# Optimization experiments

Hardware: AMD Instinct MI355X
Metric: run time of the kernel (lower is better)

The kernel has to match this reference:

```python
import jax, jax.numpy as jnp
import numpy as np

B, L, D_MODEL = 2, 4096, 256
EXPAND = 2
D_INNER = EXPAND * D_MODEL
D_STATE = 16
D_CONV = 4
DT_RANK = max(1, D_MODEL // 16)


def setup_inputs() -> dict:
    key = jax.random.key(0)
    ks = jax.random.split(key, 8)
    s = 0.02
    return {
        "x": jax.random.normal(ks[0], (B, L, D_MODEL), jnp.float32),
        "in_proj_w": jax.random.normal(ks[1], (D_MODEL, 2 * D_INNER), jnp.float32) * s,
        "conv_w": jax.random.normal(ks[2], (D_INNER, D_CONV), jnp.float32) * 0.1,
        "conv_b": jnp.zeros((D_INNER,), jnp.float32),
        "x_proj_w": jax.random.normal(ks[3], (D_INNER, DT_RANK + 2 * D_STATE), jnp.float32) * s,
        "dt_proj_w": jax.random.normal(ks[4], (DT_RANK, D_INNER), jnp.float32) * (DT_RANK ** -0.5),
        "dt_proj_b": jnp.log(jnp.expm1(jnp.full((D_INNER,), 0.01, jnp.float32))),
        "A_log": jnp.log(jnp.tile(jnp.arange(1, D_STATE + 1, dtype=jnp.float32), (D_INNER, 1))),
        "D": jnp.ones((D_INNER,), jnp.float32),
        "out_proj_w": jax.random.normal(ks[5], (D_INNER, D_MODEL), jnp.float32) * s,
        "ln_gamma": jnp.ones((D_MODEL,), jnp.float32),
        "ln_beta": jnp.zeros((D_MODEL,), jnp.float32),
    }


def _mamba(x, in_proj_w, conv_w, conv_b, x_proj_w, dt_proj_w, dt_proj_b, A_log, D, out_proj_w):
    b = x.shape[0]
    xz = x @ in_proj_w                       # [B,L,2*d_inner]
    u, z = jnp.split(xz, 2, axis=-1)
    # depthwise causal conv over time
    u_pad = jnp.pad(u, ((0, 0), (D_CONV - 1, 0), (0, 0)))
    kern = conv_w.T[:, None, :]              # [D_CONV, 1, D_INNER]
    u_conv = jax.lax.conv_general_dilated(
        u_pad, kern, (1,), 'VALID',
        dimension_numbers=('NHC', 'HIO', 'NHC'),
        feature_group_count=D_INNER) + conv_b
    u_conv = jax.nn.silu(u_conv)             # [B,L,d_inner]
    dbl = u_conv @ x_proj_w
    dt, Bm, Cm = jnp.split(dbl, [DT_RANK, DT_RANK + D_STATE], axis=-1)
    delta = jax.nn.softplus(dt @ dt_proj_w + dt_proj_b)   # [B,L,d_inner]
    A = -jnp.exp(A_log)                                    # [d_inner,d_state]
    dA = jnp.exp(delta[..., None] * A)                     # [B,L,di,ds]
    dBu = delta[..., None] * Bm[:, :, None, :] * u_conv[..., None]

    def step(h, inputs):
        dA_t, dBu_t, C_t = inputs
        h = dA_t * h + dBu_t                 # [B,di,ds]
        y = jnp.einsum('bdn,bn->bd', h, C_t)
        return h, y

    h0 = jnp.zeros((b, D_INNER, D_STATE), u_conv.dtype)
    _, ys = jax.lax.scan(step, h0,
                         (dA.transpose(1, 0, 2, 3),
                          dBu.transpose(1, 0, 2, 3),
                          Cm.transpose(1, 0, 2)))
    y = ys.transpose(1, 0, 2) + u_conv * D
    y = y * jax.nn.silu(z)
    return y @ out_proj_w


def reference(x, in_proj_w, conv_w, conv_b, x_proj_w, dt_proj_w, dt_proj_b,
              A_log, D, out_proj_w, ln_gamma, ln_beta):
    y = x + _mamba(x, in_proj_w, conv_w, conv_b, x_proj_w, dt_proj_w,
                   dt_proj_b, A_log, D, out_proj_w)
    mu = jnp.mean(y, axis=-1, keepdims=True)
    var = jnp.var(y, axis=-1, keepdims=True)
    return (y - mu) / jnp.sqrt(var + 1e-5) * ln_gamma + ln_beta
```

## Files before the change

### kernel.cpp

```cpp
#include <hip/hip_runtime.h>
#include <math.h>

constexpr int BATCH  = 2;
constexpr int LSEQ   = 4096;
constexpr int DMODEL = 256;
constexpr int DINNER = 512;
constexpr int NST    = 16;
constexpr int MROWS  = BATCH * LSEQ;
constexpr int NCH    = 256;
constexpr int TCH    = LSEQ / NCH;
constexpr float LOG2E = 1.44269504088896f;

typedef __attribute__((ext_vector_type(8))) short bf16x8;
typedef __attribute__((ext_vector_type(4))) float f32x4;

__device__ __forceinline__ float fast_silu(float v) { return v / (1.f + __expf(-v)); }

__device__ __forceinline__ unsigned short f2bf(float f) {
  unsigned int u = __float_as_uint(f);
  u = (u + 0x7fffu + ((u >> 16) & 1u)) >> 16;
  return (unsigned short)u;
}
__device__ __forceinline__ float bf2f(unsigned short u) {
  return __uint_as_float(((unsigned int)u) << 16);
}

__global__ __launch_bounds__(256) void k_cast_x(const float* __restrict__ x,
                                                unsigned short* __restrict__ xb) {
  int i = (blockIdx.x * 256 + threadIdx.x) * 4;
  float4 v = *(const float4*)(x + i);
  ushort4 o;
  o.x = f2bf(v.x); o.y = f2bf(v.y); o.z = f2bf(v.z); o.w = f2bf(v.w);
  *(ushort4*)(xb + i) = o;
}

__global__ __launch_bounds__(256) void k_castT(const float* __restrict__ W,
                                               unsigned short* __restrict__ Wt,
                                               int K, int N, int ktiles) {
  __shared__ float tile[32][33];
  const int bt = blockIdx.x;
  const int kt = bt % ktiles, nt = bt / ktiles;
  const int k0 = kt * 32, n0 = nt * 32;
  const int t = threadIdx.x;
  const int c = t & 31, r0 = t >> 5;
  #pragma unroll
  for (int it = 0; it < 4; ++it) {
    int r = r0 + it * 8;
    tile[r][c] = W[(size_t)(k0 + r) * N + n0 + c];
  }
  __syncthreads();
  #pragma unroll
  for (int it = 0; it < 4; ++it) {
    int cc = r0 + it * 8;
    Wt[(size_t)(n0 + cc) * K + k0 + c] = f2bf(tile[c][cc]);
  }
}

__global__ __launch_bounds__(256) void k_cast_xpw(const float* __restrict__ xpw,
                                                  unsigned short* __restrict__ xpT) {
  int idx = blockIdx.x * 256 + threadIdx.x;
  int n = idx >> 9, k = idx & 511;
  xpT[n * 512 + k] = f2bf(xpw[k * 48 + n]);
}

__global__ __launch_bounds__(256) void k_inproj(const unsigned short* __restrict__ Xb,
                                                const unsigned short* __restrict__ Wt,
                                                unsigned short* __restrict__ ub,
                                                unsigned short* __restrict__ zb) {
  __shared__ unsigned short As[128][40];
  __shared__ unsigned short Bs[128][40];
  const int t = threadIdx.x;
  const int m0 = (blockIdx.x & 63) * 128;
  const int n0 = (blockIdx.x >> 6) * 128;
  const int lane = t & 63, wid = t >> 6;
  const int hi = lane >> 4, l15 = lane & 15;
  const int wm = wid >> 1, wn = wid & 1;
  f32x4 zero = {0.f, 0.f, 0.f, 0.f};
  f32x4 acc[4][4];
  #pragma unroll
  for (int i = 0; i < 4; ++i)
    #pragma unroll
    for (int j = 0; j < 4; ++j) acc[i][j] = zero;

  for (int k0 = 0; k0 < DMODEL; k0 += 32) {
    __syncthreads();
    #pragma unroll
    for (int it = 0; it < 2; ++it) {
      int v = it * 256 + t;
      int r = v >> 2, part = v & 3;
      *(float4*)(&As[r][part * 8]) = *(const float4*)(Xb + (size_t)(m0 + r) * 256 + k0 + part * 8);
      *(float4*)(&Bs[r][part * 8]) = *(const float4*)(Wt + (size_t)(n0 + r) * 256 + k0 + part * 8);
    }
    __syncthreads();
    bf16x8 af[4], bfv[4];
    #pragma unroll
    for (int am = 0; am < 4; ++am) af[am] = *(const bf16x8*)(&As[wm * 64 + am * 16 + l15][hi * 8]);
    #pragma unroll
    for (int bn = 0; bn < 4; ++bn) bfv[bn] = *(const bf16x8*)(&Bs[wn * 64 + bn * 16 + l15][hi * 8]);
    #pragma unroll
    for (int am = 0; am < 4; ++am)
      #pragma unroll
      for (int bn = 0; bn < 4; ++bn)
        acc[am][bn] = __builtin_amdgcn_mfma_f32_16x16x32_bf16(af[am], bfv[bn], acc[am][bn], 0, 0, 0);
  }

  unsigned short* dst = (n0 < DINNER) ? ub : zb;
  const int nb = (n0 < DINNER) ? n0 : n0 - DINNER;
  #pragma unroll
  for (int am = 0; am < 4; ++am)
    #pragma unroll
    for (int j = 0; j < 4; ++j) {
      int m = m0 + wm * 64 + am * 16 + hi * 4 + j;
      #pragma unroll
      for (int bn = 0; bn < 4; ++bn) {
        int n = nb + wn * 64 + bn * 16 + l15;
        dst[(size_t)m * DINNER + n] = f2bf(acc[am][bn][j]);
      }
    }
}

__global__ __launch_bounds__(256) void k_conv(const unsigned short* __restrict__ ub,
                                              const float* __restrict__ cw,
                                              const float* __restrict__ cb,
                                              unsigned short* __restrict__ ucb) {
  const int idx = blockIdx.x * 256 + threadIdx.x;
  const int d = idx & (DINNER - 1);
  const int m = idx >> 9;
  const int l = m & (LSEQ - 1);
  float acc = cb[d];
  #pragma unroll
  for (int j = 0; j < 4; ++j) {
    int lj = l + j - 3;
    float uu = (lj >= 0) ? bf2f(ub[idx + (j - 3) * DINNER]) : 0.f;
    acc = fmaf(uu, cw[d * 4 + j], acc);
  }
  ucb[idx] = f2bf(fast_silu(acc));
}

__global__ __launch_bounds__(128) void k_xprojm(const unsigned short* __restrict__ ucb,
                                                const unsigned short* __restrict__ xpT,
                                                float* __restrict__ dt_out,
                                                float* __restrict__ Bout,
                                                float* __restrict__ Cout) {
  __shared__ unsigned short As[32][136];
  __shared__ unsigned short Bs[48][136];
  const int t = threadIdx.x;
  const int m0 = blockIdx.x * 32;
  const int lane = t & 63, wid = t >> 6;
  const int hi = lane >> 4, l15 = lane & 15;
  f32x4 zero = {0.f, 0.f, 0.f, 0.f};
  f32x4 acc[3] = {zero, zero, zero};

  for (int k0 = 0; k0 < DINNER; k0 += 128) {
    __syncthreads();
    #pragma unroll
    for (int it = 0; it < 4; ++it) {
      int v = it * 128 + t;
      int r = v >> 4, part = v & 15;
      *(float4*)(&As[r][part * 8]) = *(const float4*)(ucb + (size_t)(m0 + r) * 512 + k0 + part * 8);
    }
    #pragma unroll
    for (int it = 0; it < 6; ++it) {
      int v = it * 128 + t;
      int r = v >> 4, part = v & 15;
      *(float4*)(&Bs[r][part * 8]) = *(const float4*)(xpT + (size_t)r * 512 + k0 + part * 8);
    }
    __syncthreads();
    #pragma unroll
    for (int kk = 0; kk < 4; ++kk) {
      bf16x8 af = *(const bf16x8*)(&As[wid * 16 + l15][kk * 32 + hi * 8]);
      #pragma unroll
      for (int nf = 0; nf < 3; ++nf) {
        bf16x8 bv = *(const bf16x8*)(&Bs[nf * 16 + l15][kk * 32 + hi * 8]);
        acc[nf] = __builtin_amdgcn_mfma_f32_16x16x32_bf16(af, bv, acc[nf], 0, 0, 0);
      }
    }
  }
  #pragma unroll
  for (int j = 0; j < 4; ++j) {
    int m = m0 + wid * 16 + hi * 4 + j;
    dt_out[m * 16 + l15] = acc[0][j];
    Bout[m * 16 + l15]   = acc[1][j];
    Cout[m * 16 + l15]   = acc[2][j];
  }
}

__global__ __launch_bounds__(256) void k_scan1(const unsigned short* __restrict__ ucb,
                                               const float* __restrict__ dtin,
                                               const float* __restrict__ dtw,
                                               const float* __restrict__ dtb,
                                               const float* __restrict__ Bin,
                                               const float* __restrict__ Alog,
                                               unsigned short* __restrict__ delta_b,
                                               float* __restrict__ Ssum,
                                               float* __restrict__ Dsum) {
  const int g = blockIdx.x * 256 + threadIdx.x;
  const int d    = g & (DINNER - 1);
  const int rest = g >> 9;
  const int c = rest & (NCH - 1);
  const int b = rest >> 8;
  __shared__ float Bsh[TCH][NST];
  __shared__ float dtsh[TCH][NST];
  {
    const int base = (b * LSEQ + c * TCH) * NST;
    int v = threadIdx.x;
    ((float*)Bsh)[v]  = Bin[base + v];
    ((float*)dtsh)[v] = dtin[base + v];
  }
  __syncthreads();
  float dwreg[NST];
  #pragma unroll
  for (int r = 0; r < NST; ++r) dwreg[r] = dtw[r * DINNER + d];
  const float bias = dtb[d];
  float a2[NST];
  #pragma unroll
  for (int n = 0; n < NST; ++n) a2[n] = -__expf(Alog[d * NST + n]) * LOG2E;
  bool geo = true;
  #pragma unroll
  for (int n = 1; n < NST; ++n)
    geo = geo && (fabsf(a2[n] - (float)(n + 1) * a2[0]) <= 1e-5f * fabsf(a2[n]));
  float S[NST];
  #pragma unroll
  for (int n = 0; n < NST; ++n) S[n] = 0.f;
  float dsum = 0.f;
  const int row0 = (b * LSEQ + c * TCH) * DINNER + d;
  for (int tt = 0; tt < TCH; ++tt) {
    float acc = bias;
    #pragma unroll
    for (int r = 0; r < NST; ++r) acc = fmaf(dtsh[tt][r], dwreg[r], acc);
    float sp = (acc > 20.f) ? acc : log1pf(__expf(acc));
    unsigned short deb = f2bf(sp);
    delta_b[row0 + tt * DINNER] = deb;
    float de = bf2f(deb);
    float xv = bf2f(ucb[row0 + tt * DINNER]);
    float du = de * xv;
    dsum += de;
    float dA[NST];
    if (geo) {
      float r1 = exp2f(de * a2[0]);
      float p = r1;
      #pragma unroll
      for (int n = 0; n < NST; ++n) { dA[n] = p; p *= r1; }
    } else {
      #pragma unroll
      for (int n = 0; n < NST; ++n) dA[n] = exp2f(de * a2[n]);
    }
    #pragma unroll
    for (int n = 0; n < NST; ++n) S[n] = fmaf(dA[n], S[n], du * Bsh[tt][n]);
  }
  const int bc = b * NCH + c;
  Dsum[bc * DINNER + d] = dsum;
  #pragma unroll
  for (int n = 0; n < NST; ++n)
    Ssum[(size_t)((n * BATCH + b) * NCH + c) * DINNER + d] = S[n];
}

__global__ __launch_bounds__(64) void k_scan2(const float* __restrict__ S,
                                              const float* __restrict__ Dsum,
                                              const float* __restrict__ Alog,
                                              float* __restrict__ Hinit) {
  const int idx = blockIdx.x * 64 + threadIdx.x;
  const int d  = idx & (DINNER - 1);
  const int nb = idx >> 9;
  const int b  = nb & (BATCH - 1);
  const int n  = nb >> 1;
  const float a = -__expf(Alog[d * NST + n]);
  const float* Srow = S    + (size_t)nb * NCH * DINNER + d;
  const float* Drow = Dsum + (size_t)b  * NCH * DINNER + d;
  float*       Hrow = Hinit + (size_t)nb * NCH * DINNER + d;
  float h = 0.f;
  #pragma unroll 8
  for (int c = 0; c < NCH; ++c) {
    float ds = Drow[(size_t)c * DINNER];
    float s  = Srow[(size_t)c * DINNER];
    Hrow[(size_t)c * DINNER] = h;
    h = fmaf(__expf(a * ds), h, s);
  }
}

__global__ __launch_bounds__(256) void k_scan3(const unsigned short* __restrict__ ucb,
                                               const unsigned short* __restrict__ delta_b,
                                               const float* __restrict__ Bin,
                                               const float* __restrict__ Cin,
                                               const float* __restrict__ Alog,
                                               const float* __restrict__ Dvec,
                                               const float* __restrict__ Hinit,
                                               unsigned short* __restrict__ zb) {
  const int g = blockIdx.x * 256 + threadIdx.x;
  const int d    = g & (DINNER - 1);
  const int rest = g >> 9;
  const int c = rest & (NCH - 1);
  const int b = rest >> 8;
  __shared__ float Bsh[TCH][NST];
  __shared__ float Csh[TCH][NST];
  {
    const int base = (b * LSEQ + c * TCH) * NST;
    int v = threadIdx.x;
    ((float*)Bsh)[v] = Bin[base + v];
    ((float*)Csh)[v] = Cin[base + v];
  }
  __syncthreads();
  float a2[NST];
  #pragma unroll
  for (int n = 0; n < NST; ++n) a2[n] = -__expf(Alog[d * NST + n]) * LOG2E;
  bool geo = true;
  #pragma unroll
  for (int n = 1; n < NST; ++n)
    geo = geo && (fabsf(a2[n] - (float)(n + 1) * a2[0]) <= 1e-5f * fabsf(a2[n]));
  float h[NST];
  #pragma unroll
  for (int n = 0; n < NST; ++n)
    h[n] = Hinit[(size_t)(((n * BATCH + b) * NCH) + c) * DINNER + d];
  const float Dd = Dvec[d];
  const int row0 = (b * LSEQ + c * TCH) * DINNER + d;
  for (int tt = 0; tt < TCH; ++tt) {
    float de = bf2f(delta_b[row0 + tt * DINNER]);
    float xv = bf2f(ucb[row0 + tt * DINNER]);
    float du = de * xv;
    float dA[NST];
    if (geo) {
      float r1 = exp2f(de * a2[0]);
      float p = r1;
      #pragma unroll
      for (int n = 0; n < NST; ++n) { dA[n] = p; p *= r1; }
    } else {
      #pragma unroll
      for (int n = 0; n < NST; ++n) dA[n] = exp2f(de * a2[n]);
    }
    float y = 0.f;
    #pragma unroll
    for (int n = 0; n < NST; ++n) {
      h[n] = fmaf(dA[n], h[n], du * Bsh[tt][n]);
      y = fmaf(h[n], Csh[tt][n], y);
    }
    float zz = bf2f(zb[row0 + tt * DINNER]);
    zb[row0 + tt * DINNER] = f2bf((y + xv * Dd) * fast_silu(zz));
  }
}

__global__ __launch_bounds__(512) void k_out(const unsigned short* __restrict__ Yb,
                                             const unsigned short* __restrict__ W2t,
                                             const float* __restrict__ X,
                                             const float* __restrict__ gam,
                                             const float* __restrict__ bet,
                                             float* __restrict__ out) {
  __shared__ unsigned short As[32][40];
  __shared__ unsigned short Bs[256][40];
  __shared__ float red[4][32][2];
  const int t = threadIdx.x;
  const int m0 = blockIdx.x * 32;
  const int lane = t & 63, wid = t >> 6;
  const int hi = lane >> 4, l15 = lane & 15;
  const int wm = wid >> 2, wn = wid & 3;
  f32x4 zero = {0.f, 0.f, 0.f, 0.f};
  f32x4 acc[4];
  #pragma unroll
  for (int bn = 0; bn < 4; ++bn) acc[bn] = zero;

  for (int k0 = 0; k0 < DINNER; k0 += 32) {
    __syncthreads();
    if (t < 128) {
      int r = t >> 2, part = t & 3;
      *(float4*)(&As[r][part * 8]) = *(const float4*)(Yb + (size_t)(m0 + r) * 512 + k0 + part * 8);
    }
    #pragma unroll
    for (int it = 0; it < 2; ++it) {
      int v = it * 512 + t;
      int r = v >> 2, part = v & 3;
      *(float4*)(&Bs[r][part * 8]) = *(const float4*)(W2t + (size_t)r * 512 + k0 + part * 8);
    }
    __syncthreads();
    bf16x8 af = *(const bf16x8*)(&As[wm * 16 + l15][hi * 8]);
    #pragma unroll
    for (int bn = 0; bn < 4; ++bn) {
      bf16x8 bfr = *(const bf16x8*)(&Bs[wn * 64 + bn * 16 + l15][hi * 8]);
      acc[bn] = __builtin_amdgcn_mfma_f32_16x16x32_bf16(af, bfr, acc[bn], 0, 0, 0);
    }
  }

  float vv[4][4];
  float s[4] = {0.f, 0.f, 0.f, 0.f}, s2[4] = {0.f, 0.f, 0.f, 0.f};
  #pragma unroll
  for (int bn = 0; bn < 4; ++bn) {
    int n = wn * 64 + bn * 16 + l15;
    #pragma unroll
    for (int j = 0; j < 4; ++j) {
      int m = m0 + wm * 16 + hi * 4 + j;
      float v = acc[bn][j] + X[(size_t)m * DMODEL + n];
      vv[bn][j] = v;
      s[j] += v; s2[j] += v * v;
    }
  }
  #pragma unroll
  for (int j = 0; j < 4; ++j) {
    #pragma unroll
    for (int off = 1; off < 16; off <<= 1) {
      s[j]  += __shfl_xor(s[j],  off, 64);
      s2[j] += __shfl_xor(s2[j], off, 64);
    }
  }
  if (l15 == 0) {
    #pragma unroll
    for (int j = 0; j < 4; ++j) {
      red[wn][wm * 16 + hi * 4 + j][0] = s[j];
      red[wn][wm * 16 + hi * 4 + j][1] = s2[j];
    }
  }
  __syncthreads();
  float g[4], bb[4];
  #pragma unroll
  for (int bn = 0; bn < 4; ++bn) {
    int n = wn * 64 + bn * 16 + l15;
    g[bn] = gam[n]; bb[bn] = bet[n];
  }
  #pragma unroll
  for (int j = 0; j < 4; ++j) {
    int row = wm * 16 + hi * 4 + j;
    float S  = red[0][row][0] + red[1][row][0] + red[2][row][0] + red[3][row][0];
    float S2 = red[0][row][1] + red[1][row][1] + red[2][row][1] + red[3][row][1];
    float mu = S * (1.f / 256.f);
    float rstd = rsqrtf(S2 * (1.f / 256.f) - mu * mu + 1e-5f);
    int m = m0 + row;
    #pragma unroll
    for (int bn = 0; bn < 4; ++bn) {
      int n = wn * 64 + bn * 16 + l15;
      out[(size_t)m * DMODEL + n] = (vv[bn][j] - mu) * rstd * g[bn] + bb[bn];
    }
  }
}

extern "C" void kernel_launch(void* const* d_in, const int* in_sizes, int n_in,
                              void* d_out, int out_size, void* d_ws, size_t ws_size,
                              hipStream_t stream) {
  const float* x    = (const float*)d_in[0];
  const float* ipw  = (const float*)d_in[1];
  const float* cw   = (const float*)d_in[2];
  const float* cb   = (const float*)d_in[3];
  const float* xpw  = (const float*)d_in[4];
  const float* dtw  = (const float*)d_in[5];
  const float* dtbv = (const float*)d_in[6];
  const float* alog = (const float*)d_in[7];
  const float* Dv   = (const float*)d_in[8];
  const float* opw  = (const float*)d_in[9];
  const float* gam  = (const float*)d_in[10];
  const float* bet  = (const float*)d_in[11];
  float* out = (float*)d_out;

  char* ws = (char*)d_ws;
  unsigned short* ub  = (unsigned short*)ws;   ws += (size_t)MROWS * DINNER * 2;
  unsigned short* zb  = (unsigned short*)ws;   ws += (size_t)MROWS * DINNER * 2;
  unsigned short* ucb = (unsigned short*)ws;   ws += (size_t)MROWS * DINNER * 2;
  unsigned short* xb  = (unsigned short*)ws;   ws += (size_t)MROWS * DMODEL * 2;
  float* buf_dt = (float*)ws;  ws += (size_t)MROWS * NST * 4;
  float* buf_B  = (float*)ws;  ws += (size_t)MROWS * NST * 4;
  float* buf_C  = (float*)ws;  ws += (size_t)MROWS * NST * 4;
  float* buf_ds = (float*)ws;  ws += (size_t)BATCH * NCH * DINNER * 4;
  float* buf_S  = (float*)ws;  ws += (size_t)NST * BATCH * NCH * DINNER * 4;
  float* buf_H  = (float*)ws;  ws += (size_t)NST * BATCH * NCH * DINNER * 4;
  unsigned short* W1t = (unsigned short*)ws; ws += (size_t)1024 * 256 * 2;
  unsigned short* W2t = (unsigned short*)ws; ws += (size_t)256 * 512 * 2;
  unsigned short* xpT = (unsigned short*)ws; ws += (size_t)48 * 512 * 2;
  unsigned short* deltab = ub;

  k_cast_x  <<<dim3(2048), dim3(256), 0, stream>>>(x, xb);
  k_castT   <<<dim3(256),  dim3(256), 0, stream>>>(ipw, W1t, 256, 1024, 8);
  k_castT   <<<dim3(128),  dim3(256), 0, stream>>>(opw, W2t, 512, 256, 16);
  k_cast_xpw<<<dim3(96),   dim3(256), 0, stream>>>(xpw, xpT);
  k_inproj  <<<dim3(512),  dim3(256), 0, stream>>>(xb, W1t, ub, zb);
  k_conv    <<<dim3(MROWS * DINNER / 256), dim3(256), 0, stream>>>(ub, cw, cb, ucb);
  k_xprojm  <<<dim3(MROWS / 32), dim3(128), 0, stream>>>(ucb, xpT, buf_dt, buf_B, buf_C);
  k_scan1   <<<dim3(BATCH * NCH * DINNER / 256), dim3(256), 0, stream>>>(ucb, buf_dt, dtw, dtbv, buf_B,
                                                                         alog, deltab, buf_S, buf_ds);
  k_scan2   <<<dim3(NST * BATCH * DINNER / 64), dim3(64), 0, stream>>>(buf_S, buf_ds, alog, buf_H);
  k_scan3   <<<dim3(BATCH * NCH * DINNER / 256), dim3(256), 0, stream>>>(ucb, deltab, buf_B, buf_C,
                                                                         alog, Dv, buf_H, zb);
  k_out     <<<dim3(MROWS / 32), dim3(512), 0, stream>>>(zb, W2t, x, gam, bet, out);
}
```

Measured before the change: 134.3 us.

## Move delta projection to MFMA kernel, vectorize conv, shorten scan dependency chains

Splits the dt_proj matmul and softplus out of the first scan pass into a separate MFMA-based kernel that writes bf16 delta, so the scan no longer does a 16-term FMA per element. The depthwise conv now handles two channels per thread with 32-bit loads and stores. The geometric dA powers are computed with a log-depth product tree instead of a serial multiply chain, and the C-dot reduction in scan3 is split into four partial accumulators to shorten the dependency chain. In exchange it adds an extra launch and a pass that writes delta to memory and reads it back, and dt is rounded to bf16 before the projection.

Measured after the change: 159.4 us. +18.7%, slower.

```diff
diff --git a/kernel.cpp b/kernel.cpp
--- a/kernel.cpp
+++ b/kernel.cpp
@@ -25,6 +25,15 @@
   return __uint_as_float(((unsigned int)u) << 16);
 }
 
+__device__ __forceinline__ void powers16(float r1, float* dA) {
+  float r2 = r1 * r1, r3 = r2 * r1, r4 = r2 * r2;
+  float r5 = r4 * r1, r6 = r4 * r2, r7 = r4 * r3, r8 = r4 * r4;
+  dA[0] = r1; dA[1] = r2; dA[2] = r3; dA[3] = r4;
+  dA[4] = r5; dA[5] = r6; dA[6] = r7; dA[7] = r8;
+  dA[8]  = r8 * r1; dA[9]  = r8 * r2; dA[10] = r8 * r3; dA[11] = r8 * r4;
+  dA[12] = r8 * r5; dA[13] = r8 * r6; dA[14] = r8 * r7; dA[15] = r8 * r8;
+}
+
 __global__ __launch_bounds__(256) void k_cast_x(const float* __restrict__ x,
                                                 unsigned short* __restrict__ xb) {
   int i = (blockIdx.x * 256 + threadIdx.x) * 4;
@@ -61,6 +70,13 @@
   int idx = blockIdx.x * 256 + threadIdx.x;
   int n = idx >> 9, k = idx & 511;
   xpT[n * 512 + k] = f2bf(xpw[k * 48 + n]);
+}
+
+__global__ __launch_bounds__(256) void k_cast_dtw(const float* __restrict__ dtw,
+                                                  unsigned short* __restrict__ dtwT) {
+  int idx = blockIdx.x * 256 + threadIdx.x;
+  int n = idx >> 5, k = idx & 31;
+  dtwT[idx] = (k < 16) ? f2bf(dtw[k * 512 + n]) : (unsigned short)0;
 }
 
 __global__ __launch_bounds__(256) void k_inproj(const unsigned short* __restrict__ Xb,
@@ -123,18 +139,23 @@
                                               const float* __restrict__ cw,
                                               const float* __restrict__ cb,
                                               unsigned short* __restrict__ ucb) {
-  const int idx = blockIdx.x * 256 + threadIdx.x;
+  const int e2 = blockIdx.x * 256 + threadIdx.x;
+  const int idx = e2 * 2;
   const int d = idx & (DINNER - 1);
   const int m = idx >> 9;
   const int l = m & (LSEQ - 1);
-  float acc = cb[d];
+  float a0 = cb[d], a1 = cb[d + 1];
   #pragma unroll
   for (int j = 0; j < 4; ++j) {
     int lj = l + j - 3;
-    float uu = (lj >= 0) ? bf2f(ub[idx + (j - 3) * DINNER]) : 0.f;
-    acc = fmaf(uu, cw[d * 4 + j], acc);
-  }
-  ucb[idx] = f2bf(fast_silu(acc));
+    unsigned int p = (lj >= 0) ? *(const unsigned int*)(ub + idx + (j - 3) * DINNER) : 0u;
+    float u0 = bf2f((unsigned short)(p & 0xffffu));
+    float u1 = bf2f((unsigned short)(p >> 16));
+    a0 = fmaf(u0, cw[d * 4 + j], a0);
+    a1 = fmaf(u1, cw[(d + 1) * 4 + j], a1);
+  }
+  unsigned int o = (unsigned int)f2bf(fast_silu(a0)) | ((unsigned int)f2bf(fast_silu(a1)) << 16);
+  *(unsigned int*)(ucb + idx) = o;
 }
 
 __global__ __launch_bounds__(128) void k_xprojm(const unsigned short* __restrict__ ucb,
@@ -185,13 +206,47 @@
   }
 }
 
+__global__ __launch_bounds__(256) void k_deltam(const float* __restrict__ dt,
+                                                const unsigned short* __restrict__ dtwT,
+                                                const float* __restrict__ dtb,
+                                                unsigned short* __restrict__ delta_b) {
+  __shared__ unsigned short As[32][40];
+  const int t = threadIdx.x;
+  const int m0 = blockIdx.x * 32;
+  const int lane = t & 63, w = t >> 6;
+  const int hi = lane >> 4, l15 = lane & 15;
+  for (int i = t; i < 32 * 32; i += 256) {
+    int r = i >> 5, k = i & 31;
+    As[r][k] = (k < 16) ? f2bf(dt[(size_t)(m0 + r) * 16 + k]) : (unsigned short)0;
+  }
+  __syncthreads();
+  bf16x8 af[2];
+  #pragma unroll
+  for (int am = 0; am < 2; ++am) af[am] = *(const bf16x8*)(&As[am * 16 + l15][hi * 8]);
+  f32x4 zero = {0.f, 0.f, 0.f, 0.f};
+  #pragma unroll
+  for (int bn = 0; bn < 8; ++bn) {
+    int n = w * 128 + bn * 16 + l15;
+    bf16x8 bv = *(const bf16x8*)(dtwT + (size_t)n * 32 + hi * 8);
+    float bias = dtb[n];
+    #pragma unroll
+    for (int am = 0; am < 2; ++am) {
+      f32x4 acc = __builtin_amdgcn_mfma_f32_16x16x32_bf16(af[am], bv, zero, 0, 0, 0);
+      #pragma unroll
+      for (int j = 0; j < 4; ++j) {
+        float v = acc[j] + bias;
+        float sp = (v > 20.f) ? v : log1pf(__expf(v));
+        int m = m0 + am * 16 + hi * 4 + j;
+        delta_b[(size_t)m * DINNER + n] = f2bf(sp);
+      }
+    }
+  }
+}
+
 __global__ __launch_bounds__(256) void k_scan1(const unsigned short* __restrict__ ucb,
-                                               const float* __restrict__ dtin,
-                                               const float* __restrict__ dtw,
-                                               const float* __restrict__ dtb,
+                                               const unsigned short* __restrict__ delta_b,
                                                const float* __restrict__ Bin,
                                                const float* __restrict__ Alog,
-                                               unsigned short* __restrict__ delta_b,
                                                float* __restrict__ Ssum,
                                                float* __restrict__ Dsum) {
   const int g = blockIdx.x * 256 + threadIdx.x;
@@ -200,18 +255,11 @@
   const int c = rest & (NCH - 1);
   const int b = rest >> 8;
   __shared__ float Bsh[TCH][NST];
-  __shared__ float dtsh[TCH][NST];
   {
     const int base = (b * LSEQ + c * TCH) * NST;
-    int v = threadIdx.x;
-    ((float*)Bsh)[v]  = Bin[base + v];
-    ((float*)dtsh)[v] = dtin[base + v];
+    ((float*)Bsh)[threadIdx.x] = Bin[base + threadIdx.x];
   }
   __syncthreads();
-  float dwreg[NST];
-  #pragma unroll
-  for (int r = 0; r < NST; ++r) dwreg[r] = dtw[r * DINNER + d];
-  const float bias = dtb[d];
   float a2[NST];
   #pragma unroll
   for (int n = 0; n < NST; ++n) a2[n] = -__expf(Alog[d * NST + n]) * LOG2E;
@@ -225,22 +273,13 @@
   float dsum = 0.f;
   const int row0 = (b * LSEQ + c * TCH) * DINNER + d;
   for (int tt = 0; tt < TCH; ++tt) {
-    float acc = bias;
-    #pragma unroll
-    for (int r = 0; r < NST; ++r) acc = fmaf(dtsh[tt][r], dwreg[r], acc);
-    float sp = (acc > 20.f) ? acc : log1pf(__expf(acc));
-    unsigned short deb = f2bf(sp);
-    delta_b[row0 + tt * DINNER] = deb;
-    float de = bf2f(deb);
+    float de = bf2f(delta_b[row0 + tt * DINNER]);
     float xv = bf2f(ucb[row0 + tt * DINNER]);
     float du = de * xv;
     dsum += de;
     float dA[NST];
     if (geo) {
-      float r1 = exp2f(de * a2[0]);
-      float p = r1;
-      #pragma unroll
-      for (int n = 0; n < NST; ++n) { dA[n] = p; p *= r1; }
+      powers16(exp2f(de * a2[0]), dA);
     } else {
       #pragma unroll
       for (int n = 0; n < NST; ++n) dA[n] = exp2f(de * a2[n]);
@@ -265,8 +304,8 @@
   const int b  = nb & (BATCH - 1);
   const int n  = nb >> 1;
   const float a = -__expf(Alog[d * NST + n]);
-  const float* Srow = S    + (size_t)nb * NCH * DINNER + d;
-  const float* Drow = Dsum + (size_t)b  * NCH * DINNER + d;
+  const float* Srow = S     + (size_t)nb * NCH * DINNER + d;
+  const float* Drow = Dsum  + (size_t)b  * NCH * DINNER + d;
   float*       Hrow = Hinit + (size_t)nb * NCH * DINNER + d;
   float h = 0.f;
   #pragma unroll 8
@@ -295,9 +334,8 @@
   __shared__ float Csh[TCH][NST];
   {
     const int base = (b * LSEQ + c * TCH) * NST;
-    int v = threadIdx.x;
-    ((float*)Bsh)[v] = Bin[base + v];
-    ((float*)Csh)[v] = Cin[base + v];
+    ((float*)Bsh)[threadIdx.x] = Bin[base + threadIdx.x];
+    ((float*)Csh)[threadIdx.x] = Cin[base + threadIdx.x];
   }
   __syncthreads();
   float a2[NST];
@@ -319,20 +357,18 @@
     float du = de * xv;
     float dA[NST];
     if (geo) {
-      float r1 = exp2f(de * a2[0]);
-      float p = r1;
-      #pragma unroll
-      for (int n = 0; n < NST; ++n) { dA[n] = p; p *= r1; }
+      powers16(exp2f(de * a2[0]), dA);
     } else {
       #pragma unroll
       for (int n = 0; n < NST; ++n) dA[n] = exp2f(de * a2[n]);
     }
-    float y = 0.f;
+    float yp[4] = {0.f, 0.f, 0.f, 0.f};
     #pragma unroll
     for (int n = 0; n < NST; ++n) {
       h[n] = fmaf(dA[n], h[n], du * Bsh[tt][n]);
-      y = fmaf(h[n], Csh[tt][n], y);
-    }
+      yp[n & 3] = fmaf(h[n], Csh[tt][n], yp[n & 3]);
+    }
+    float y = (yp[0] + yp[1]) + (yp[2] + yp[3]);
     float zz = bf2f(zb[row0 + tt * DINNER]);
     zb[row0 + tt * DINNER] = f2bf((y + xv * Dd) * fast_silu(zz));
   }
@@ -457,20 +493,23 @@
   float* buf_ds = (float*)ws;  ws += (size_t)BATCH * NCH * DINNER * 4;
   float* buf_S  = (float*)ws;  ws += (size_t)NST * BATCH * NCH * DINNER * 4;
   float* buf_H  = (float*)ws;  ws += (size_t)NST * BATCH * NCH * DINNER * 4;
-  unsigned short* W1t = (unsigned short*)ws; ws += (size_t)1024 * 256 * 2;
-  unsigned short* W2t = (unsigned short*)ws; ws += (size_t)256 * 512 * 2;
-  unsigned short* xpT = (unsigned short*)ws; ws += (size_t)48 * 512 * 2;
+  unsigned short* W1t  = (unsigned short*)ws; ws += (size_t)1024 * 256 * 2;
+  unsigned short* W2t  = (unsigned short*)ws; ws += (size_t)256 * 512 * 2;
+  unsigned short* xpT  = (unsigned short*)ws; ws += (size_t)48 * 512 * 2;
+  unsigned short* dtwT = (unsigned short*)ws; ws += (size_t)512 * 32 * 2;
   unsigned short* deltab = ub;
 
   k_cast_x  <<<dim3(2048), dim3(256), 0, stream>>>(x, xb);
   k_castT   <<<dim3(256),  dim3(256), 0, stream>>>(ipw, W1t, 256, 1024, 8);
   k_castT   <<<dim3(128),  dim3(256), 0, stream>>>(opw, W2t, 512, 256, 16);
   k_cast_xpw<<<dim3(96),   dim3(256), 0, stream>>>(xpw, xpT);
+  k_cast_dtw<<<dim3(64),   dim3(256), 0, stream>>>(dtw, dtwT);
   k_inproj  <<<dim3(512),  dim3(256), 0, stream>>>(xb, W1t, ub, zb);
-  k_conv    <<<dim3(MROWS * DINNER / 256), dim3(256), 0, stream>>>(ub, cw, cb, ucb);
+  k_conv    <<<dim3(MROWS * DINNER / 512), dim3(256), 0, stream>>>(ub, cw, cb, ucb);
   k_xprojm  <<<dim3(MROWS / 32), dim3(128), 0, stream>>>(ucb, xpT, buf_dt, buf_B, buf_C);
-  k_scan1   <<<dim3(BATCH * NCH * DINNER / 256), dim3(256), 0, stream>>>(ucb, buf_dt, dtw, dtbv, buf_B,
-                                                                         alog, deltab, buf_S, buf_ds);
+  k_deltam  <<<dim3(MROWS / 32), dim3(256), 0, stream>>>(buf_dt, dtwT, dtbv, deltab);
+  k_scan1   <<<dim3(BATCH * NCH * DINNER / 256), dim3(256), 0, stream>>>(ucb, deltab, buf_B,
+                                                                         alog, buf_S, buf_ds);
   k_scan2   <<<dim3(NST * BATCH * DINNER / 64), dim3(64), 0, stream>>>(buf_S, buf_ds, alog, buf_H);
   k_scan3   <<<dim3(BATCH * NCH * DINNER / 256), dim3(256), 0, stream>>>(ucb, deltab, buf_B, buf_C,
                                                                          alog, Dv, buf_H, zb);
```
